# Kernel tuning notes

Hardware: AMD Instinct MI355X
Metric: run time of the kernel (lower is better)

The kernel has to match this reference:

```python
import jax, jax.numpy as jnp
import numpy as np

N_NODES = 50000


def _gcn_conv(x, W, b, edge_index, num_nodes):
    # PyG GCNConv defaults: add self loops, symmetric normalization.
    h = x @ W  # [N, out]
    loop = jnp.arange(num_nodes, dtype=edge_index.dtype)
    src = jnp.concatenate([edge_index[0], loop])  # [E+N]
    dst = jnp.concatenate([edge_index[1], loop])
    ones = jnp.ones(src.shape[0], dtype=x.dtype)
    deg = jax.ops.segment_sum(ones, dst, num_segments=num_nodes)  # in-degree incl. self loop
    dinv = jnp.where(deg > 0, jax.lax.rsqrt(deg), 0.0)
    norm = dinv[src] * dinv[dst]  # [E+N]
    msgs = h[src] * norm[:, None]  # gather + scale (memory-bound)
    out = jax.ops.segment_sum(msgs, dst, num_segments=num_nodes)
    return out + b


def setup_inputs() -> dict:
    key = jax.random.key(0)
    k1, k2, k3, k4 = jax.random.split(key, 4)
    F_in, H = 128, 16
    x = jax.random.normal(k1, (N_NODES, F_in), dtype=jnp.float32)
    edge_index = jax.random.randint(k2, (2, 800000), 0, N_NODES, dtype=jnp.int64)
    # Glorot-ish init for weights
    W1 = jax.random.normal(k3, (F_in, H), dtype=jnp.float32) / np.sqrt(F_in)
    W2 = jax.random.normal(k4, (H, F_in), dtype=jnp.float32) / np.sqrt(H)
    b1 = jnp.zeros((H,), dtype=jnp.float32)
    b2 = jnp.zeros((F_in,), dtype=jnp.float32)
    return {"x": x, "edge_index": edge_index, "W1": W1, "b1": b1, "W2": W2, "b2": b2}


def reference(x, edge_index, W1, b1, W2, b2):
    h = jax.nn.relu(_gcn_conv(x, W1, b1, edge_index, N_NODES))
    out = _gcn_conv(h, W2, b2, edge_index, N_NODES)
    return out
```

## Files before the change

kernel.cpp:

```cpp
#include <hip/hip_runtime.h>

#define N_NODES 50000
#define NPB 128
#define NBUCKET ((N_NODES + NPB - 1) / NPB)
#define CAP 2816
#define CHUNK 4096
#define EPT 8
#define G1_NPB 32
#define NG1 ((N_NODES + G1_NPB - 1) / G1_NPB)
#define NCHUNK ((800000 + CHUNK - 1) / CHUNK)


__global__ __launch_bounds__(512) void k_partgemm1(const int* __restrict__ src,
                                                   const int* __restrict__ dst,
                                                   int* __restrict__ gcursor,
                                                   int* __restrict__ ewords, int E,
                                                   const float* __restrict__ x,
                                                   const float* __restrict__ W1,
                                                   float* __restrict__ h1) {
    __shared__ __align__(16) char smem[25344 + 64];
    int tid = threadIdx.x;

    if (blockIdx.x < NCHUNK) {
        int* words  = (int*)smem;
        int* hist   = (int*)(smem + 16384);
        int* lstart = (int*)(smem + 16384 + 2048);
        int* gbase  = (int*)(smem + 16384 + 4096);
        int* wsum   = (int*)(smem + 16384 + 6144);

        int cbase = blockIdx.x * CHUNK;
        int count = min(CHUNK, E - cbase);

        hist[tid] = 0;
        __syncthreads();

        int w[EPT];
        if (cbase + CHUNK <= E) {
#pragma unroll
            for (int hh = 0; hh < 2; hh++) {
                int4 s4 = ((const int4*)(src + cbase))[tid + 512 * hh];
                int4 d4 = ((const int4*)(dst + cbase))[tid + 512 * hh];
                int ss[4] = {s4.x, s4.y, s4.z, s4.w};
                int dd[4] = {d4.x, d4.y, d4.z, d4.w};
#pragma unroll
                for (int c = 0; c < 4; c++) {
                    int b = dd[c] >> 7;
                    w[hh * 4 + c] = ss[c] | ((dd[c] & 127) << 16) | (b << 23);
                    atomicAdd(&hist[b], 1);
                }
            }
        } else {
#pragma unroll
            for (int r = 0; r < EPT; r++) {
                int i = tid * EPT + r;
                if (i < count) {
                    int s = src[cbase + i];
                    int d = dst[cbase + i];
                    int b = d >> 7;
                    w[r] = s | ((d & 127) << 16) | (b << 23);
                    atomicAdd(&hist[b], 1);
                } else {
                    w[r] = -1;
                }
            }
        }
        __syncthreads();

        int h = hist[tid];
        int lane = tid & 63;
        int v = h;
#pragma unroll
        for (int off = 1; off < 64; off <<= 1) {
            int t = __shfl_up(v, off, 64);
            if (lane >= off) v += t;
        }
        if (lane == 63) wsum[tid >> 6] = v;
        __syncthreads();
        int woff = 0;
        int wv = tid >> 6;
        for (int i = 0; i < wv; i++) woff += wsum[i];
        int excl = v + woff - h;
        hist[tid] = excl;
        lstart[tid] = excl;
        __syncthreads();

#pragma unroll
        for (int r = 0; r < EPT; r++) {
            if (w[r] != -1) {
                int b = ((unsigned)w[r]) >> 23;
                int pos = atomicAdd(&hist[b], 1);
                words[pos] = w[r];
            }
        }
        __syncthreads();

        if (tid < NBUCKET) {
            int nb = hist[tid] - lstart[tid];
            gbase[tid] = (nb > 0) ? atomicAdd(&gcursor[tid], nb) : 0;
        }
        __syncthreads();

        for (int i = tid; i < count; i += 512) {
            int ww = words[i];
            int b = ((unsigned)ww) >> 23;
            ewords[b * CAP + gbase[b] + (i - lstart[b])] = ww;
        }
    } else {
        float* sx  = (float*)smem;
        float* swT = sx + 32 * 132;
        int n0 = (blockIdx.x - NCHUNK) * G1_NPB;

        {
            float4 v = ((const float4*)W1)[tid];
            int k = tid >> 2;
            int j4 = (tid & 3) << 2;
            swT[(j4 + 0) * 132 + k] = v.x;
            swT[(j4 + 1) * 132 + k] = v.y;
            swT[(j4 + 2) * 132 + k] = v.z;
            swT[(j4 + 3) * 132 + k] = v.w;
        }
        const float4* x4 = (const float4*)(x + (size_t)n0 * 128);
#pragma unroll
        for (int r = 0; r < 2; r++) {
            int q = tid + 512 * r;
            int row = q >> 5;
            if (n0 + row < N_NODES) {
                float4 v = x4[q];
                int k = (q & 31) << 2;
                *(float4*)&sx[row * 132 + k] = v;
            }
        }
        __syncthreads();

        int node = tid >> 4;
        int j = tid & 15;
        float acc = 0.f;
#pragma unroll
        for (int k = 0; k < 128; k += 4) {
            float4 a = *(const float4*)&sx[node * 132 + k];
            float4 bb = *(const float4*)&swT[j * 132 + k];
            acc = fmaf(a.x, bb.x, acc);
            acc = fmaf(a.y, bb.y, acc);
            acc = fmaf(a.z, bb.z, acc);
            acc = fmaf(a.w, bb.w, acc);
        }
        int n = n0 + node;
        if (n < N_NODES) h1[(size_t)n * 16 + j] = acc;
    }
}


__global__ __launch_bounds__(512) void k_sortscale(const int* __restrict__ ewords,
                                                   const int* __restrict__ gcursor,
                                                   unsigned short* __restrict__ eidx,
                                                   int* __restrict__ row_start,
                                                   int* __restrict__ deg,
                                                   float* __restrict__ dinv,
                                                   float* __restrict__ h1) {
    __shared__ unsigned short sorted[CAP];
    __shared__ int hist[NPB];
    __shared__ int sc[NPB];
    __shared__ float sdinv[NPB];
    int tid = threadIdx.x;
    int b = blockIdx.x;
    int base = b * CAP;
    int count = gcursor[b];

    if (tid < NPB) hist[tid] = 0;
    __syncthreads();

    int w[(CAP + 511) / 512];
#pragma unroll
    for (int r = 0; r < (CAP + 511) / 512; r++) {
        int i = tid + 512 * r;
        if (i < count) {
            int ww = ewords[base + i];
            w[r] = ww;
            atomicAdd(&hist[(ww >> 16) & 127], 1);
        } else {
            w[r] = -1;
        }
    }
    __syncthreads();

    int v = 0;
    if (tid < NPB) { v = hist[tid]; sc[tid] = v; }
    __syncthreads();
    for (int off = 1; off < NPB; off <<= 1) {
        int t = 0;
        if (tid < NPB && tid >= off) t = sc[tid - off];
        __syncthreads();
        if (tid < NPB) sc[tid] += t;
        __syncthreads();
    }
    if (tid < NPB) {
        int excl = sc[tid] - v;
        int node = b * NPB + tid;
        float dv = rsqrtf((float)(v + 1));
        sdinv[tid] = dv;
        if (node < N_NODES) {
            row_start[node] = base + excl;
            deg[node] = v;
            dinv[node] = dv;
        }
        hist[tid] = excl;
    }
    __syncthreads();

#pragma unroll
    for (int r = 0; r < (CAP + 511) / 512; r++) {
        if (w[r] != -1) {
            int ldst = (w[r] >> 16) & 127;
            int pos = atomicAdd(&hist[ldst], 1);
            sorted[pos] = (unsigned short)(w[r] & 0xFFFF);
        }
    }
    __syncthreads();

    for (int i = tid; i < count; i += 512) eidx[base + i] = sorted[i];

    float4* h4 = (float4*)(h1 + (size_t)b * NPB * 16);
    int nvalid4 = (b == NBUCKET - 1) ? (N_NODES - b * NPB) * 4 : NPB * 4;
    if (tid < nvalid4) {
        float dv = sdinv[tid >> 2];
        float4 vv = h4[tid];
        vv.x *= dv; vv.y *= dv; vv.z *= dv; vv.w *= dv;
        h4[tid] = vv;
    }
}


__global__ __launch_bounds__(256) void k_agg1(const float* __restrict__ h1s,
                                              const int* __restrict__ row_start,
                                              const int* __restrict__ deg,
                                              const unsigned short* __restrict__ eidx,
                                              const float* __restrict__ dinv,
                                              const float* __restrict__ b1,
                                              float* __restrict__ z1s) {
    int lane = threadIdx.x & 63;
    int node = blockIdx.x * 4 + (threadIdx.x >> 6);
    int f = lane & 15;
    int sub = lane >> 4;

    int start = row_start[node];
    int d = deg[node];
    int m = min(d, 64);

    int e = 0;
    if (m > 0) e = (int)eidx[start + min(lane, m - 1)];

    float a0 = 0.f, a1 = 0.f;
    int iters = (m + 7) >> 3;
    int i = sub;
    for (int t = 0; t < iters; t++, i += 8) {
        int s0 = __shfl(e, min(i, m - 1), 64);
        int s1 = __shfl(e, min(i + 4, m - 1), 64);
        float v0 = h1s[s0 * 16 + f];
        float v1 = h1s[s1 * 16 + f];
        if (i < m) a0 += v0;
        if (i + 4 < m) a1 += v1;
    }
    for (int q = 64 + sub; q < d; q += 4)
        a0 += h1s[(int)eidx[start + q] * 16 + f];
    float acc = a0 + a1;

    acc += __shfl_xor(acc, 16, 64);
    acc += __shfl_xor(acc, 32, 64);
    acc += h1s[node * 16 + f];

    float dv = dinv[node];
    float z = fmaxf(fmaf(dv, acc, b1[f]), 0.f);
    if (sub == 0) z1s[node * 16 + f] = dv * z;
}


__global__ __launch_bounds__(512) void k_aggmm(const float* __restrict__ z1s,
                                               const int* __restrict__ row_start,
                                               const int* __restrict__ deg,
                                               const unsigned short* __restrict__ eidx,
                                               const float* __restrict__ dinv,
                                               const float* __restrict__ W2,
                                               const float* __restrict__ b2,
                                               float* __restrict__ out) {
    __shared__ float sw2[16 * 128];
    __shared__ float sb2[128];
    int tid = threadIdx.x;

    ((float4*)sw2)[tid] = ((const float4*)W2)[tid];
    if (tid < 32) ((float4*)sb2)[tid] = ((const float4*)b2)[tid];
    __syncthreads();

    int lane = tid & 63;
    int node = blockIdx.x * 8 + (tid >> 6);
    int f = lane & 15;
    int sub = lane >> 4;

    int start = row_start[node];
    int d = deg[node];
    int m = min(d, 64);

    int e = 0;
    if (m > 0) e = (int)eidx[start + min(lane, m - 1)];

    float a0 = 0.f, a1 = 0.f;
    int iters = (m + 7) >> 3;
    int i = sub;
    for (int u = 0; u < iters; u++, i += 8) {
        int s0 = __shfl(e, min(i, m - 1), 64);
        int s1 = __shfl(e, min(i + 4, m - 1), 64);
        float v0 = z1s[s0 * 16 + f];
        float v1 = z1s[s1 * 16 + f];
        if (i < m) a0 += v0;
        if (i + 4 < m) a1 += v1;
    }
    for (int q = 64 + sub; q < d; q += 4)
        a0 += z1s[(int)eidx[start + q] * 16 + f];
    float acc = a0 + a1;

    acc += __shfl_xor(acc, 16, 64);
    acc += __shfl_xor(acc, 32, 64);
    acc += z1s[node * 16 + f];
    float s2 = dinv[node] * acc;

    float o0 = sb2[lane];
    float o1 = sb2[lane + 64];
#pragma unroll
    for (int k = 0; k < 16; k++) {
        float sk = __shfl(s2, k, 64);
        o0 = fmaf(sk, sw2[k * 128 + lane], o0);
        o1 = fmaf(sk, sw2[k * 128 + 64 + lane], o1);
    }
    out[(size_t)node * 128 + lane] = o0;
    out[(size_t)node * 128 + 64 + lane] = o1;
}


extern "C" void kernel_launch(void* const* d_in, const int* in_sizes, int n_in,
                              void* d_out, int out_size, void* d_ws, size_t ws_size,
                              hipStream_t stream) {
    const float* x  = (const float*)d_in[0];
    const int*   ei = (const int*)d_in[1];
    const float* W1 = (const float*)d_in[2];
    const float* b1 = (const float*)d_in[3];
    const float* W2 = (const float*)d_in[4];
    const float* b2 = (const float*)d_in[5];
    float* out = (float*)d_out;

    const int E = in_sizes[1] / 2;
    const int* src = ei;
    const int* dst = ei + E;

    char* ws = (char*)d_ws;
    int*            gcursor   = (int*)(ws + 0);
    int*            ewords    = (int*)(ws + 2048);
    float*          h1        = (float*)(ws + 4406272);
    unsigned short* eidx      = (unsigned short*)(ws + 7606272);
    int*            row_start = (int*)(ws + 9808384);
    int*            deg       = (int*)(ws + 10008384);
    float*          dinv      = (float*)(ws + 10208384);
    float*          z1s       = (float*)(ws + 10408384);

    hipMemsetAsync(gcursor, 0, NBUCKET * sizeof(int), stream);
    k_partgemm1<<<NCHUNK + NG1, 512, 0, stream>>>(src, dst, gcursor, ewords, E, x, W1, h1);
    k_sortscale<<<NBUCKET, 512, 0, stream>>>(ewords, gcursor, eidx, row_start, deg, dinv, h1);
    k_agg1<<<N_NODES / 4, 256, 0, stream>>>(h1, row_start, deg, eidx, dinv, b1, z1s);
    k_aggmm<<<N_NODES / 8, 512, 0, stream>>>(z1s, row_start, deg, eidx, dinv, W2, b2, out);
}
```

Before: 150.2 us.

## Fuse all GCN stages into one persistent cooperative kernel with grid syncs

Replaces the memset and four separate kernel launches with a single cooperative persistent kernel that zeroes the cursors, partitions edges, runs the first GEMM, sorts buckets, and performs both aggregations, separated by grid-wide barriers. Blocks loop over jobs using a grid-stride pattern, and the grid size comes from an occupancy query capped at 512 blocks. This targets launch overhead and inter-kernel gaps. In exchange it adds grid-sync cost, caps parallelism at 512 blocks per phase, and may lower occupancy because of the larger shared-memory and register footprint.

```diff
diff --git a/kernel.cpp b/kernel.cpp
--- a/kernel.cpp
+++ b/kernel.cpp
@@ -1,4 +1,7 @@
 #include <hip/hip_runtime.h>
+#include <hip/hip_cooperative_groups.h>
+
+namespace cg = cooperative_groups;
 
 #define N_NODES 50000
 #define NPB 128
@@ -9,346 +12,347 @@
 #define G1_NPB 32
 #define NG1 ((N_NODES + G1_NPB - 1) / G1_NPB)
 #define NCHUNK ((800000 + CHUNK - 1) / CHUNK)
-
-
-__global__ __launch_bounds__(512) void k_partgemm1(const int* __restrict__ src,
-                                                   const int* __restrict__ dst,
-                                                   int* __restrict__ gcursor,
-                                                   int* __restrict__ ewords, int E,
-                                                   const float* __restrict__ x,
-                                                   const float* __restrict__ W1,
-                                                   float* __restrict__ h1) {
-    __shared__ __align__(16) char smem[25344 + 64];
+#define MAXBLK 512
+
+
+__global__ __launch_bounds__(512, 4) void k_fused(
+    const int* __restrict__ src, const int* __restrict__ dst,
+    const float* __restrict__ x, const float* __restrict__ W1,
+    const float* __restrict__ b1, const float* __restrict__ W2,
+    const float* __restrict__ b2, float* __restrict__ out,
+    int* __restrict__ gcursor, int* __restrict__ ewords,
+    float* __restrict__ h1, unsigned short* __restrict__ eidx,
+    int* __restrict__ row_start, int* __restrict__ deg,
+    float* __restrict__ dinv, float* __restrict__ z1s, int E) {
+
+    cg::grid_group grid = cg::this_grid();
+    __shared__ __align__(16) char smem[25408];
     int tid = threadIdx.x;
-
-    if (blockIdx.x < NCHUNK) {
-        int* words  = (int*)smem;
-        int* hist   = (int*)(smem + 16384);
-        int* lstart = (int*)(smem + 16384 + 2048);
-        int* gbase  = (int*)(smem + 16384 + 4096);
-        int* wsum   = (int*)(smem + 16384 + 6144);
-
-        int cbase = blockIdx.x * CHUNK;
-        int count = min(CHUNK, E - cbase);
-
-        hist[tid] = 0;
-        __syncthreads();
-
-        int w[EPT];
-        if (cbase + CHUNK <= E) {
-#pragma unroll
-            for (int hh = 0; hh < 2; hh++) {
-                int4 s4 = ((const int4*)(src + cbase))[tid + 512 * hh];
-                int4 d4 = ((const int4*)(dst + cbase))[tid + 512 * hh];
-                int ss[4] = {s4.x, s4.y, s4.z, s4.w};
-                int dd[4] = {d4.x, d4.y, d4.z, d4.w};
-#pragma unroll
-                for (int c = 0; c < 4; c++) {
-                    int b = dd[c] >> 7;
-                    w[hh * 4 + c] = ss[c] | ((dd[c] & 127) << 16) | (b << 23);
-                    atomicAdd(&hist[b], 1);
-                }
-            }
-        } else {
-#pragma unroll
-            for (int r = 0; r < EPT; r++) {
-                int i = tid * EPT + r;
+    int blk = blockIdx.x;
+    int nblk = gridDim.x;
+    int lane = tid & 63;
+
+    for (int i = blk * 512 + tid; i < NBUCKET; i += nblk * 512) gcursor[i] = 0;
+    grid.sync();
+
+    {
+        int njobs = NCHUNK + NG1;
+        for (int job = blk; job < njobs; job += nblk) {
+            __syncthreads();
+            if (job < NCHUNK) {
+                int* words  = (int*)smem;
+                int* hist   = (int*)(smem + 16384);
+                int* lstart = (int*)(smem + 18432);
+                int* gbase  = (int*)(smem + 20480);
+                int* wsum   = (int*)(smem + 22528);
+
+                int cbase = job * CHUNK;
+                int count = min(CHUNK, E - cbase);
+
+                hist[tid] = 0;
+                __syncthreads();
+
+                int w[EPT];
+                if (cbase + CHUNK <= E) {
+#pragma unroll
+                    for (int hh = 0; hh < 2; hh++) {
+                        int4 s4 = ((const int4*)(src + cbase))[tid + 512 * hh];
+                        int4 d4 = ((const int4*)(dst + cbase))[tid + 512 * hh];
+                        int ss[4] = {s4.x, s4.y, s4.z, s4.w};
+                        int dd[4] = {d4.x, d4.y, d4.z, d4.w};
+#pragma unroll
+                        for (int c = 0; c < 4; c++) {
+                            int b = dd[c] >> 7;
+                            w[hh * 4 + c] = ss[c] | ((dd[c] & 127) << 16) | (b << 23);
+                            atomicAdd(&hist[b], 1);
+                        }
+                    }
+                } else {
+#pragma unroll
+                    for (int r = 0; r < EPT; r++) {
+                        int i = tid * EPT + r;
+                        if (i < count) {
+                            int s = src[cbase + i];
+                            int d = dst[cbase + i];
+                            int b = d >> 7;
+                            w[r] = s | ((d & 127) << 16) | (b << 23);
+                            atomicAdd(&hist[b], 1);
+                        } else {
+                            w[r] = -1;
+                        }
+                    }
+                }
+                __syncthreads();
+
+                int h = hist[tid];
+                int v = h;
+#pragma unroll
+                for (int off = 1; off < 64; off <<= 1) {
+                    int t = __shfl_up(v, off, 64);
+                    if (lane >= off) v += t;
+                }
+                if (lane == 63) wsum[tid >> 6] = v;
+                __syncthreads();
+                int woff = 0;
+                int wv = tid >> 6;
+                for (int i = 0; i < wv; i++) woff += wsum[i];
+                int excl = v + woff - h;
+                hist[tid] = excl;
+                lstart[tid] = excl;
+                __syncthreads();
+
+#pragma unroll
+                for (int r = 0; r < EPT; r++) {
+                    if (w[r] != -1) {
+                        int b = ((unsigned)w[r]) >> 23;
+                        int pos = atomicAdd(&hist[b], 1);
+                        words[pos] = w[r];
+                    }
+                }
+                __syncthreads();
+
+                if (tid < NBUCKET) {
+                    int nb = hist[tid] - lstart[tid];
+                    gbase[tid] = (nb > 0) ? atomicAdd(&gcursor[tid], nb) : 0;
+                }
+                __syncthreads();
+
+                for (int i = tid; i < count; i += 512) {
+                    int ww = words[i];
+                    int b = ((unsigned)ww) >> 23;
+                    ewords[b * CAP + gbase[b] + (i - lstart[b])] = ww;
+                }
+            } else {
+                float* sx  = (float*)smem;
+                float* swT = sx + 32 * 132;
+                int n0 = (job - NCHUNK) * G1_NPB;
+
+                {
+                    float4 v = ((const float4*)W1)[tid];
+                    int k = tid >> 2;
+                    int j4 = (tid & 3) << 2;
+                    swT[(j4 + 0) * 132 + k] = v.x;
+                    swT[(j4 + 1) * 132 + k] = v.y;
+                    swT[(j4 + 2) * 132 + k] = v.z;
+                    swT[(j4 + 3) * 132 + k] = v.w;
+                }
+                const float4* x4 = (const float4*)(x + (size_t)n0 * 128);
+#pragma unroll
+                for (int r = 0; r < 2; r++) {
+                    int q = tid + 512 * r;
+                    int row = q >> 5;
+                    if (n0 + row < N_NODES) {
+                        float4 v = x4[q];
+                        int k = (q & 31) << 2;
+                        *(float4*)&sx[row * 132 + k] = v;
+                    }
+                }
+                __syncthreads();
+
+                int node = tid >> 4;
+                int j = tid & 15;
+                float acc = 0.f;
+#pragma unroll
+                for (int k = 0; k < 128; k += 4) {
+                    float4 a = *(const float4*)&sx[node * 132 + k];
+                    float4 bb = *(const float4*)&swT[j * 132 + k];
+                    acc = fmaf(a.x, bb.x, acc);
+                    acc = fmaf(a.y, bb.y, acc);
+                    acc = fmaf(a.z, bb.z, acc);
+                    acc = fmaf(a.w, bb.w, acc);
+                }
+                int n = n0 + node;
+                if (n < N_NODES) h1[(size_t)n * 16 + j] = acc;
+            }
+        }
+    }
+    grid.sync();
+
+    {
+        unsigned short* sorted = (unsigned short*)smem;
+        int*   hist  = (int*)(smem + 5632);
+        int*   sc    = (int*)(smem + 6144);
+        float* sdinv = (float*)(smem + 6656);
+
+        for (int b = blk; b < NBUCKET; b += nblk) {
+            __syncthreads();
+            int base = b * CAP;
+            int count = gcursor[b];
+
+            if (tid < NPB) hist[tid] = 0;
+            __syncthreads();
+
+            int w[(CAP + 511) / 512];
+#pragma unroll
+            for (int r = 0; r < (CAP + 511) / 512; r++) {
+                int i = tid + 512 * r;
                 if (i < count) {
-                    int s = src[cbase + i];
-                    int d = dst[cbase + i];
-                    int b = d >> 7;
-                    w[r] = s | ((d & 127) << 16) | (b << 23);
-                    atomicAdd(&hist[b], 1);
+                    int ww = ewords[base + i];
+                    w[r] = ww;
+                    atomicAdd(&hist[(ww >> 16) & 127], 1);
                 } else {
                     w[r] = -1;
                 }
             }
-        }
-        __syncthreads();
-
-        int h = hist[tid];
-        int lane = tid & 63;
-        int v = h;
-#pragma unroll
-        for (int off = 1; off < 64; off <<= 1) {
-            int t = __shfl_up(v, off, 64);
-            if (lane >= off) v += t;
-        }
-        if (lane == 63) wsum[tid >> 6] = v;
-        __syncthreads();
-        int woff = 0;
-        int wv = tid >> 6;
-        for (int i = 0; i < wv; i++) woff += wsum[i];
-        int excl = v + woff - h;
-        hist[tid] = excl;
-        lstart[tid] = excl;
-        __syncthreads();
-
-#pragma unroll
-        for (int r = 0; r < EPT; r++) {
-            if (w[r] != -1) {
-                int b = ((unsigned)w[r]) >> 23;
-                int pos = atomicAdd(&hist[b], 1);
-                words[pos] = w[r];
-            }
-        }
-        __syncthreads();
-
-        if (tid < NBUCKET) {
-            int nb = hist[tid] - lstart[tid];
-            gbase[tid] = (nb > 0) ? atomicAdd(&gcursor[tid], nb) : 0;
-        }
-        __syncthreads();
-
-        for (int i = tid; i < count; i += 512) {
-            int ww = words[i];
-            int b = ((unsigned)ww) >> 23;
-            ewords[b * CAP + gbase[b] + (i - lstart[b])] = ww;
-        }
-    } else {
-        float* sx  = (float*)smem;
-        float* swT = sx + 32 * 132;
-        int n0 = (blockIdx.x - NCHUNK) * G1_NPB;
-
-        {
-            float4 v = ((const float4*)W1)[tid];
-            int k = tid >> 2;
-            int j4 = (tid & 3) << 2;
-            swT[(j4 + 0) * 132 + k] = v.x;
-            swT[(j4 + 1) * 132 + k] = v.y;
-            swT[(j4 + 2) * 132 + k] = v.z;
-            swT[(j4 + 3) * 132 + k] = v.w;
-        }
-        const float4* x4 = (const float4*)(x + (size_t)n0 * 128);
-#pragma unroll
-        for (int r = 0; r < 2; r++) {
-            int q = tid + 512 * r;
-            int row = q >> 5;
-            if (n0 + row < N_NODES) {
-                float4 v = x4[q];
-                int k = (q & 31) << 2;
-                *(float4*)&sx[row * 132 + k] = v;
-            }
-        }
-        __syncthreads();
-
-        int node = tid >> 4;
-        int j = tid & 15;
-        float acc = 0.f;
-#pragma unroll
-        for (int k = 0; k < 128; k += 4) {
-            float4 a = *(const float4*)&sx[node * 132 + k];
-            float4 bb = *(const float4*)&swT[j * 132 + k];
-            acc = fmaf(a.x, bb.x, acc);
-            acc = fmaf(a.y, bb.y, acc);
-            acc = fmaf(a.z, bb.z, acc);
-            acc = fmaf(a.w, bb.w, acc);
-        }
-        int n = n0 + node;
-        if (n < N_NODES) h1[(size_t)n * 16 + j] = acc;
-    }
-}
-
-
-__global__ __launch_bounds__(512) void k_sortscale(const int* __restrict__ ewords,
-                                                   const int* __restrict__ gcursor,
-                                                   unsigned short* __restrict__ eidx,
-                                                   int* __restrict__ row_start,
-                                                   int* __restrict__ deg,
-                                                   float* __restrict__ dinv,
-                                                   float* __restrict__ h1) {
-    __shared__ unsigned short sorted[CAP];
-    __shared__ int hist[NPB];
-    __shared__ int sc[NPB];
-    __shared__ float sdinv[NPB];
-    int tid = threadIdx.x;
-    int b = blockIdx.x;
-    int base = b * CAP;
-    int count = gcursor[b];
-
-    if (tid < NPB) hist[tid] = 0;
-    __syncthreads();
-
-    int w[(CAP + 511) / 512];
-#pragma unroll
-    for (int r = 0; r < (CAP + 511) / 512; r++) {
-        int i = tid + 512 * r;
-        if (i < count) {
-            int ww = ewords[base + i];
-            w[r] = ww;
-            atomicAdd(&hist[(ww >> 16) & 127], 1);
-        } else {
-            w[r] = -1;
+            __syncthreads();
+
+            int v = 0;
+            if (tid < NPB) { v = hist[tid]; sc[tid] = v; }
+            __syncthreads();
+            for (int off = 1; off < NPB; off <<= 1) {
+                int t = 0;
+                if (tid < NPB && tid >= off) t = sc[tid - off];
+                __syncthreads();
+                if (tid < NPB) sc[tid] += t;
+                __syncthreads();
+            }
+            if (tid < NPB) {
+                int excl = sc[tid] - v;
+                int node = b * NPB + tid;
+                float dv = rsqrtf((float)(v + 1));
+                sdinv[tid] = dv;
+                if (node < N_NODES) {
+                    row_start[node] = base + excl;
+                    deg[node] = v;
+                    dinv[node] = dv;
+                }
+                hist[tid] = excl;
+            }
+            __syncthreads();
+
+#pragma unroll
+            for (int r = 0; r < (CAP + 511) / 512; r++) {
+                if (w[r] != -1) {
+                    int ldst = (w[r] >> 16) & 127;
+                    int pos = atomicAdd(&hist[ldst], 1);
+                    sorted[pos] = (unsigned short)(w[r] & 0xFFFF);
+                }
+            }
+            __syncthreads();
+
+            for (int i = tid; i < count; i += 512) eidx[base + i] = sorted[i];
+
+            float4* h4 = (float4*)(h1 + (size_t)b * NPB * 16);
+            int nvalid4 = (b == NBUCKET - 1) ? (N_NODES - b * NPB) * 4 : NPB * 4;
+            if (tid < nvalid4) {
+                float dv = sdinv[tid >> 2];
+                float4 vv = h4[tid];
+                vv.x *= dv; vv.y *= dv; vv.z *= dv; vv.w *= dv;
+                h4[tid] = vv;
+            }
         }
     }
-    __syncthreads();
-
-    int v = 0;
-    if (tid < NPB) { v = hist[tid]; sc[tid] = v; }
-    __syncthreads();
-    for (int off = 1; off < NPB; off <<= 1) {
-        int t = 0;
-        if (tid < NPB && tid >= off) t = sc[tid - off];
-        __syncthreads();
-        if (tid < NPB) sc[tid] += t;
-        __syncthreads();
-    }
-    if (tid < NPB) {
-        int excl = sc[tid] - v;
-        int node = b * NPB + tid;
-        float dv = rsqrtf((float)(v + 1));
-        sdinv[tid] = dv;
-        if (node < N_NODES) {
-            row_start[node] = base + excl;
-            deg[node] = v;
-            dinv[node] = dv;
-        }
-        hist[tid] = excl;
-    }
-    __syncthreads();
-
-#pragma unroll
-    for (int r = 0; r < (CAP + 511) / 512; r++) {
-        if (w[r] != -1) {
-            int ldst = (w[r] >> 16) & 127;
-            int pos = atomicAdd(&hist[ldst], 1);
-            sorted[pos] = (unsigned short)(w[r] & 0xFFFF);
+    grid.sync();
+
+    {
+        int f = lane & 15;
+        int sub = lane >> 4;
+        int wid = blk * 8 + (tid >> 6);
+        int wstride = nblk * 8;
+
+        for (int node = wid; node < N_NODES; node += wstride) {
+            int start = row_start[node];
+            int d = deg[node];
+            int m = min(d, 64);
+
+            int e = 0;
+            if (m > 0) e = (int)eidx[start + min(lane, m - 1)];
+
+            float a0 = 0.f, a1 = 0.f;
+            int iters = (m + 7) >> 3;
+            int i = sub;
+            for (int t = 0; t < iters; t++, i += 8) {
+                int s0 = __shfl(e, min(i, m - 1), 64);
+                int s1 = __shfl(e, min(i + 4, m - 1), 64);
+                float v0 = h1[s0 * 16 + f];
+                float v1 = h1[s1 * 16 + f];
+                if (i < m) a0 += v0;
+                if (i + 4 < m) a1 += v1;
+            }
+            for (int q = 64 + sub; q < d; q += 4)
+                a0 += h1[(int)eidx[start + q] * 16 + f];
+            float acc = a0 + a1;
+
+            acc += __shfl_xor(acc, 16, 64);
+            acc += __shfl_xor(acc, 32, 64);
+            acc += h1[node * 16 + f];
+
+            float dv = dinv[node];
+            float z = fmaxf(fmaf(dv, acc, b1[f]), 0.f);
+            if (sub == 0) z1s[node * 16 + f] = dv * z;
         }
     }
-    __syncthreads();
-
-    for (int i = tid; i < count; i += 512) eidx[base + i] = sorted[i];
-
-    float4* h4 = (float4*)(h1 + (size_t)b * NPB * 16);
-    int nvalid4 = (b == NBUCKET - 1) ? (N_NODES - b * NPB) * 4 : NPB * 4;
-    if (tid < nvalid4) {
-        float dv = sdinv[tid >> 2];
-        float4 vv = h4[tid];
-        vv.x *= dv; vv.y *= dv; vv.z *= dv; vv.w *= dv;
-        h4[tid] = vv;
+    grid.sync();
+
+    {
+        float* sw2 = (float*)smem;
+        float* sb2 = (float*)(smem + 8192);
+        __syncthreads();
+        ((float4*)sw2)[tid] = ((const float4*)W2)[tid];
+        if (tid < 32) ((float4*)sb2)[tid] = ((const float4*)b2)[tid];
+        __syncthreads();
+
+        int f = lane & 15;
+        int sub = lane >> 4;
+        int wid = blk * 8 + (tid >> 6);
+        int wstride = nblk * 8;
+
+        for (int node = wid; node < N_NODES; node += wstride) {
+            int start = row_start[node];
+            int d = deg[node];
+            int m = min(d, 64);
+
+            int e = 0;
+            if (m > 0) e = (int)eidx[start + min(lane, m - 1)];
+
+            float a0 = 0.f, a1 = 0.f;
+            int iters = (m + 7) >> 3;
+            int i = sub;
+            for (int u = 0; u < iters; u++, i += 8) {
+                int s0 = __shfl(e, min(i, m - 1), 64);
+                int s1 = __shfl(e, min(i + 4, m - 1), 64);
+                float v0 = z1s[s0 * 16 + f];
+                float v1 = z1s[s1 * 16 + f];
+                if (i < m) a0 += v0;
+                if (i + 4 < m) a1 += v1;
+            }
+            for (int q = 64 + sub; q < d; q += 4)
+                a0 += z1s[(int)eidx[start + q] * 16 + f];
+            float acc = a0 + a1;
+
+            acc += __shfl_xor(acc, 16, 64);
+            acc += __shfl_xor(acc, 32, 64);
+            acc += z1s[node * 16 + f];
+            float s2 = dinv[node] * acc;
+
+            float o0 = sb2[lane];
+            float o1 = sb2[lane + 64];
+#pragma unroll
+            for (int k = 0; k < 16; k++) {
+                float sk = __shfl(s2, k, 64);
+                o0 = fmaf(sk, sw2[k * 128 + lane], o0);
+                o1 = fmaf(sk, sw2[k * 128 + 64 + lane], o1);
+            }
+            out[(size_t)node * 128 + lane] = o0;
+            out[(size_t)node * 128 + 64 + lane] = o1;
+        }
     }
-}
-
-
-__global__ __launch_bounds__(256) void k_agg1(const float* __restrict__ h1s,
-                                              const int* __restrict__ row_start,
-                                              const int* __restrict__ deg,
-                                              const unsigned short* __restrict__ eidx,
-                                              const float* __restrict__ dinv,
-                                              const float* __restrict__ b1,
-                                              float* __restrict__ z1s) {
-    int lane = threadIdx.x & 63;
-    int node = blockIdx.x * 4 + (threadIdx.x >> 6);
-    int f = lane & 15;
-    int sub = lane >> 4;
-
-    int start = row_start[node];
-    int d = deg[node];
-    int m = min(d, 64);
-
-    int e = 0;
-    if (m > 0) e = (int)eidx[start + min(lane, m - 1)];
-
-    float a0 = 0.f, a1 = 0.f;
-    int iters = (m + 7) >> 3;
-    int i = sub;
-    for (int t = 0; t < iters; t++, i += 8) {
-        int s0 = __shfl(e, min(i, m - 1), 64);
-        int s1 = __shfl(e, min(i + 4, m - 1), 64);
-        float v0 = h1s[s0 * 16 + f];
-        float v1 = h1s[s1 * 16 + f];
-        if (i < m) a0 += v0;
-        if (i + 4 < m) a1 += v1;
-    }
-    for (int q = 64 + sub; q < d; q += 4)
-        a0 += h1s[(int)eidx[start + q] * 16 + f];
-    float acc = a0 + a1;
-
-    acc += __shfl_xor(acc, 16, 64);
-    acc += __shfl_xor(acc, 32, 64);
-    acc += h1s[node * 16 + f];
-
-    float dv = dinv[node];
-    float z = fmaxf(fmaf(dv, acc, b1[f]), 0.f);
-    if (sub == 0) z1s[node * 16 + f] = dv * z;
-}
-
-
-__global__ __launch_bounds__(512) void k_aggmm(const float* __restrict__ z1s,
-                                               const int* __restrict__ row_start,
-                                               const int* __restrict__ deg,
-                                               const unsigned short* __restrict__ eidx,
-                                               const float* __restrict__ dinv,
-                                               const float* __restrict__ W2,
-                                               const float* __restrict__ b2,
-                                               float* __restrict__ out) {
-    __shared__ float sw2[16 * 128];
-    __shared__ float sb2[128];
-    int tid = threadIdx.x;
-
-    ((float4*)sw2)[tid] = ((const float4*)W2)[tid];
-    if (tid < 32) ((float4*)sb2)[tid] = ((const float4*)b2)[tid];
-    __syncthreads();
-
-    int lane = tid & 63;
-    int node = blockIdx.x * 8 + (tid >> 6);
-    int f = lane & 15;
-    int sub = lane >> 4;
-
-    int start = row_start[node];
-    int d = deg[node];
-    int m = min(d, 64);
-
-    int e = 0;
-    if (m > 0) e = (int)eidx[start + min(lane, m - 1)];
-
-    float a0 = 0.f, a1 = 0.f;
-    int iters = (m + 7) >> 3;
-    int i = sub;
-    for (int u = 0; u < iters; u++, i += 8) {
-        int s0 = __shfl(e, min(i, m - 1), 64);
-        int s1 = __shfl(e, min(i + 4, m - 1), 64);
-        float v0 = z1s[s0 * 16 + f];
-        float v1 = z1s[s1 * 16 + f];
-        if (i < m) a0 += v0;
-        if (i + 4 < m) a1 += v1;
-    }
-    for (int q = 64 + sub; q < d; q += 4)
-        a0 += z1s[(int)eidx[start + q] * 16 + f];
-    float acc = a0 + a1;
-
-    acc += __shfl_xor(acc, 16, 64);
-    acc += __shfl_xor(acc, 32, 64);
-    acc += z1s[node * 16 + f];
-    float s2 = dinv[node] * acc;
-
-    float o0 = sb2[lane];
-    float o1 = sb2[lane + 64];
-#pragma unroll
-    for (int k = 0; k < 16; k++) {
-        float sk = __shfl(s2, k, 64);
-        o0 = fmaf(sk, sw2[k * 128 + lane], o0);
-        o1 = fmaf(sk, sw2[k * 128 + 64 + lane], o1);
-    }
-    out[(size_t)node * 128 + lane] = o0;
-    out[(size_t)node * 128 + 64 + lane] = o1;
 }
 
 
 extern "C" void kernel_launch(void* const* d_in, const int* in_sizes, int n_in,
                               void* d_out, int out_size, void* d_ws, size_t ws_size,
                               hipStream_t stream) {
-    const float* x  = (const float*)d_in[0];
-    const int*   ei = (const int*)d_in[1];
-    const float* W1 = (const float*)d_in[2];
-    const float* b1 = (const float*)d_in[3];
-    const float* W2 = (const float*)d_in[4];
-    const float* b2 = (const float*)d_in[5];
+    const int*   src = (const int*)d_in[1];
+    const float* x   = (const float*)d_in[0];
+    const float* W1  = (const float*)d_in[2];
+    const float* b1  = (const float*)d_in[3];
+    const float* W2  = (const float*)d_in[4];
+    const float* b2  = (const float*)d_in[5];
     float* out = (float*)d_out;
 
-    const int E = in_sizes[1] / 2;
-    const int* src = ei;
-    const int* dst = ei + E;
+    int E = in_sizes[1] / 2;
+    const int* dst = src + E;
 
     char* ws = (char*)d_ws;
     int*            gcursor   = (int*)(ws + 0);
@@ -360,9 +364,17 @@
     float*          dinv      = (float*)(ws + 10208384);
     float*          z1s       = (float*)(ws + 10408384);
 
-    hipMemsetAsync(gcursor, 0, NBUCKET * sizeof(int), stream);
-    k_partgemm1<<<NCHUNK + NG1, 512, 0, stream>>>(src, dst, gcursor, ewords, E, x, W1, h1);
-    k_sortscale<<<NBUCKET, 512, 0, stream>>>(ewords, gcursor, eidx, row_start, deg, dinv, h1);
-    k_agg1<<<N_NODES / 4, 256, 0, stream>>>(h1, row_start, deg, eidx, dinv, b1, z1s);
-    k_aggmm<<<N_NODES / 8, 512, 0, stream>>>(z1s, row_start, deg, eidx, dinv, W2, b2, out);
+    int maxb = 0;
+    if (hipOccupancyMaxActiveBlocksPerMultiprocessor(&maxb, k_fused, 512, 0) != hipSuccess
+        || maxb < 1) maxb = 1;
+    int nblk = maxb * 256;
+    if (nblk > MAXBLK) nblk = MAXBLK;
+
+    void* args[] = {
+        (void*)&src, (void*)&dst, (void*)&x, (void*)&W1, (void*)&b1,
+        (void*)&W2, (void*)&b2, (void*)&out,
+        (void*)&gcursor, (void*)&ewords, (void*)&h1, (void*)&eidx,
+        (void*)&row_start, (void*)&deg, (void*)&dinv, (void*)&z1s, (void*)&E
+    };
+    hipLaunchCooperativeKernel((void*)k_fused, dim3(nblk), dim3(512), args, 0, stream);
 }
```

New measurement: 324.2 us. 2.16x slower.
